# Performance work log

Hardware: AMD Instinct MI355X
Metric: run time of the kernel (lower is better)

The kernel has to match this reference:

```python
import jax, jax.numpy as jnp
import numpy as np

NEG_SLOPE = 0.2
N, E, NNZ, IN, H, C = 100000, 50000, 800000, 128, 8, 16


def setup_inputs() -> dict:
    key = jax.random.key(0)
    ks = jax.random.split(key, 8)
    X = jax.random.normal(ks[0], (N, IN), jnp.float32)
    W_typed = jax.random.normal(ks[1], (4, IN, H * C), jnp.float32) * (1.0 / np.sqrt(IN))
    att_e = jax.random.normal(ks[2], (4, H, C), jnp.float32) * 0.1
    att_v = jax.random.normal(ks[3], (4, H, C), jnp.float32) * 0.1
    vertex = jax.random.randint(ks[4], (NNZ,), 0, N, jnp.int32)
    edges = jax.random.randint(ks[5], (NNZ,), 0, E, jnp.int32)
    vtype = jax.random.randint(ks[6], (N,), 0, 4, jnp.int32)
    etype = jax.random.randint(ks[7], (E,), 0, 4, jnp.int32)
    return {"X": X, "W_typed": W_typed, "att_e": att_e, "att_v": att_v,
            "vertex": vertex, "edges": edges, "vtype": vtype, "etype": etype}


def _segment_softmax(logits, seg, num):
    # numerically-stable softmax over segments (PyG-style, eps in denominator)
    m = jax.ops.segment_max(logits, seg, num_segments=num)
    ex = jnp.exp(logits - m[seg])
    s = jax.ops.segment_sum(ex, seg, num_segments=num)
    return ex / (s[seg] + 1e-16)


def reference(X, W_typed, att_e, att_v, vertex, edges, vtype, etype):
    # typed linear: project with all 4 type weights, select per node type
    Xall = jnp.einsum('ni,tio->tno', X, W_typed)        # [4, N, H*C]
    X0 = Xall[vtype, jnp.arange(N)]                     # [N, H*C]
    Xn = X0.reshape(N, H, C)
    Xve = Xn[vertex]                                    # [NNZ, H, C] gather vertex->incidence
    # vertex->edge attention, typed by edge type of each incidence
    beta = jnp.sum(Xve * att_e[etype[edges]], axis=-1)  # [NNZ, H]
    beta = jax.nn.leaky_relu(beta, NEG_SLOPE)
    beta = _segment_softmax(beta, edges, E)
    Xe = jax.nn.relu(jax.ops.segment_sum(Xve * beta[..., None], edges, num_segments=E))  # [E, H, C]
    Xe = Xe[edges]                                      # [NNZ, H, C] gather edge->incidence
    # edge->vertex attention, typed by node type of each incidence's vertex
    alpha = jnp.sum(Xe * att_v[vtype[vertex]], axis=-1)  # [NNZ, H]
    alpha = jax.nn.leaky_relu(alpha, NEG_SLOPE)
    alpha = _segment_softmax(alpha, vertex, N)
    Xv = jax.ops.segment_sum(Xe * alpha[..., None], vertex, num_segments=N)  # [N, H, C]
    return Xv.reshape(N, H * C)
```

## Files before the change

kernel.cpp:

```cpp
#include <hip/hip_runtime.h>

typedef __attribute__((ext_vector_type(8))) short bf16x8;
typedef __attribute__((ext_vector_type(4))) float f32x4;

#define NEG_SLOPE 0.2f

__device__ __forceinline__ unsigned short f2bf(float f){
  unsigned u = __float_as_uint(f);
  u = (u + 0x7fffu + ((u >> 16) & 1u)) >> 16;
  return (unsigned short)u;
}
__device__ __forceinline__ float bflo(unsigned u){ return __uint_as_float(u << 16); }
__device__ __forceinline__ float bfhi(unsigned u){ return __uint_as_float(u & 0xffff0000u); }
__device__ __forceinline__ float lrelu(float x){ return x > 0.f ? x : NEG_SLOPE * x; }

__global__ __launch_bounds__(256) void k_prep(
    const int* __restrict__ vtype, int N, int* __restrict__ tcnt, int nbHN,
    const float* __restrict__ W, short* __restrict__ Bfrag){
  __shared__ int lcnt[4];
  int b = (int)blockIdx.x;
  if (b < nbHN){
    if (threadIdx.x < 4) lcnt[threadIdx.x] = 0;
    __syncthreads();
    int i = b * 256 + threadIdx.x;
    if (i < N) atomicAdd(&lcnt[vtype[i]], 1);
    __syncthreads();
    if (threadIdx.x < 4 && lcnt[threadIdx.x] > 0)
      atomicAdd(tcnt + threadIdx.x, lcnt[threadIdx.x]);
    return;
  }
  b -= nbHN;
  int u = b * 256 + threadIdx.x;
  int j = u & 7, lane = (u >> 3) & 63, ct = (u >> 9) & 31, ks = u >> 14;
  int k = ks * 32 + ((lane >> 4) << 3) + j;
  int col = (ct << 4) + (lane & 15);
  int t = col >> 7, o = col & 127;
  Bfrag[u] = (short)f2bf(W[(t * 128 + k) * 128 + o]);
}

__global__ void k_pbase(const int* __restrict__ tcnt, int* __restrict__ pbase){
  if (threadIdx.x == 0 && blockIdx.x == 0){
    int pb = 0;
    for (int t = 0; t < 4; ++t){
      pbase[t] = pb;
      pb += ((tcnt[t] + 63) >> 6) << 6;
    }
    pbase[4] = pb;
  }
}

__global__ __launch_bounds__(256) void k_nodeplace(
    const int* __restrict__ vtype, int N, const int* __restrict__ pbase,
    int* __restrict__ tcur, int* __restrict__ nsorted){
  __shared__ int lcnt[4];
  __shared__ int gbase[4];
  int t = threadIdx.x;
  if (t < 4) lcnt[t] = 0;
  __syncthreads();
  int i = (int)blockIdx.x * 256 + t;
  int tt = 0, rank = 0;
  bool valid = i < N;
  if (valid){ tt = vtype[i]; rank = atomicAdd(&lcnt[tt], 1); }
  __syncthreads();
  if (t < 4 && lcnt[t] > 0) gbase[t] = atomicAdd(tcur + t, lcnt[t]);
  __syncthreads();
  if (valid) nsorted[pbase[tt] + gbase[tt] + rank] = i;
}

__global__ __launch_bounds__(256, 3) void k_gemm_hist(const float* __restrict__ X,
    const short* __restrict__ Bfrag, const int* __restrict__ nsorted,
    const int* __restrict__ pbase, unsigned short* __restrict__ X0,
    const int* __restrict__ edges, const int* __restrict__ vertex, int NNZ,
    int* __restrict__ cnt, int E,
    int* __restrict__ rank_e, int* __restrict__ rank_v, int nbHist4){
  __shared__ short shB[8 * 4 * 64 * 8];
  const int tid = threadIdx.x;
  const int q = (int)blockIdx.x / 3, r = (int)blockIdx.x % 3;

  if (r != 0){
    int hb = 2 * q + (r - 1);
    if (hb < nbHist4){
      int i0 = hb * 1024 + tid;
      #pragma unroll
      for (int k = 0; k < 4; ++k){
        int i = i0 + k * 256;
        if (i < NNZ){
          rank_e[i] = atomicAdd(cnt + edges[i], 1);
          rank_v[i] = atomicAdd(cnt + E + vertex[i], 1);
        }
      }
    }
    return;
  }

  const int rowIdx = q * 64;
  const int t = (rowIdx >= pbase[1]) + (rowIdx >= pbase[2]) + (rowIdx >= pbase[3]);

  const bf16x8* Bv = (const bf16x8*)Bfrag;
  bf16x8* shBv = (bf16x8*)shB;
  #pragma unroll
  for (int v = 0; v < 8; ++v){
    int item = v * 256 + tid;
    int slab = item >> 6, ln = item & 63;
    int ks = slab >> 3, ctl = slab & 7;
    shBv[item] = Bv[((ks * 32 + 8 * t + ctl) * 64) + ln];
  }

  const int w = tid >> 6, lane = tid & 63;
  const int m = lane & 15, qq = lane >> 4;
  const int node = nsorted[rowIdx + w * 16 + m];

  bf16x8 afrag[4];
  #pragma unroll
  for (int ks = 0; ks < 4; ++ks){
    bf16x8 f;
    if (node >= 0){
      const float4* src = (const float4*)(X + (size_t)node * 128 + ks * 32 + qq * 8);
      float4 a = src[0], b = src[1];
      f[0]=(short)f2bf(a.x); f[1]=(short)f2bf(a.y); f[2]=(short)f2bf(a.z); f[3]=(short)f2bf(a.w);
      f[4]=(short)f2bf(b.x); f[5]=(short)f2bf(b.y); f[6]=(short)f2bf(b.z); f[7]=(short)f2bf(b.w);
    } else {
      #pragma unroll
      for (int z = 0; z < 8; ++z) f[z] = 0;
    }
    afrag[ks] = f;
  }

  f32x4 acc[8];
  #pragma unroll
  for (int ct = 0; ct < 8; ++ct){
    acc[ct][0]=0.f; acc[ct][1]=0.f; acc[ct][2]=0.f; acc[ct][3]=0.f;
  }

  __syncthreads();
  #pragma unroll
  for (int ctl = 0; ctl < 8; ++ctl){
    #pragma unroll
    for (int ks = 0; ks < 4; ++ks){
      bf16x8 bf = shBv[(ks * 8 + ctl) * 64 + lane];
      acc[ctl] = __builtin_amdgcn_mfma_f32_16x16x32_bf16(afrag[ks], bf, acc[ctl], 0, 0, 0);
    }
  }

  const int col0 = lane & 15;
  #pragma unroll
  for (int rr = 0; rr < 4; ++rr){
    int row = nsorted[rowIdx + w * 16 + qq * 4 + rr];
    if (row < 0) continue;
    #pragma unroll
    for (int ctl = 0; ctl < 8; ++ctl)
      X0[(size_t)row * 128 + ctl * 16 + col0] = f2bf(acc[ctl][rr]);
  }
}

__global__ __launch_bounds__(256) void k_scanA(const int* __restrict__ cnt, int S,
                                               int* __restrict__ bsum){
  __shared__ int sh[256];
  int base = blockIdx.x * 1024 + threadIdx.x * 4;
  int s = 0;
  #pragma unroll
  for (int k = 0; k < 4; ++k){ int idx = base + k; if (idx < S) s += cnt[idx]; }
  sh[threadIdx.x] = s; __syncthreads();
  for (int off = 128; off > 0; off >>= 1){
    if (threadIdx.x < off) sh[threadIdx.x] += sh[threadIdx.x + off];
    __syncthreads();
  }
  if (threadIdx.x == 0) bsum[blockIdx.x] = sh[0];
}

__global__ __launch_bounds__(256) void k_scanC3(const int* __restrict__ cnt, int S,
    const int* __restrict__ bsum, int nb, int* __restrict__ offs){
  __shared__ int shb[256];
  __shared__ int sh[256];
  int t = threadIdx.x;
  int b = (int)blockIdx.x;
  shb[t] = (t < nb) ? bsum[t] : 0;
  __syncthreads();
  for (int off = 1; off < 256; off <<= 1){
    int v = (t >= off) ? shb[t - off] : 0; __syncthreads();
    shb[t] += v; __syncthreads();
  }
  int bbase = (b == 0) ? 0 : shb[b - 1];
  int base = b * 1024 + t * 4;
  int c[4]; int s = 0;
  #pragma unroll
  for (int k = 0; k < 4; ++k){ int idx = base + k; c[k] = (idx < S) ? cnt[idx] : 0; s += c[k]; }
  sh[t] = s; __syncthreads();
  for (int off = 1; off < 256; off <<= 1){
    int v = (t >= off) ? sh[t - off] : 0; __syncthreads();
    sh[t] += v; __syncthreads();
  }
  int run = bbase + sh[t] - s;
  #pragma unroll
  for (int k = 0; k < 4; ++k){
    int idx = base + k;
    if (idx < S){ offs[idx] = run; run += c[k]; }
  }
}

__global__ __launch_bounds__(256) void k_place(
    const int* __restrict__ edges, const int* __restrict__ vertex, int NNZ,
    const int* __restrict__ offs, const int* __restrict__ rank_e,
    const int* __restrict__ rank_v, int* __restrict__ rows, int E){
  int q = (int)blockIdx.x >> 1, r = (int)blockIdx.x & 1;
  int i = q * 256 + (int)threadIdx.x;
  if (i >= NNZ) return;
  if (r == 0) rows[offs[edges[i]]      + rank_e[i]] = vertex[i];
  else        rows[offs[E + vertex[i]] + rank_v[i]] = edges[i];
}

template<int OUT_BF16>
__device__ __forceinline__ void seg_body(const uint4* __restrict__ feat,
    const float* __restrict__ att, const int* __restrict__ rows_sorted,
    const int* __restrict__ offs, const int* __restrict__ cnt,
    const int* __restrict__ stype, void* __restrict__ outbuf,
    int S, int blockId, int tid){
  int wid = tid >> 6, lane = tid & 63;
  int s = blockId * 4 + wid;
  if (s >= S) return;
  int t = stype[s];
  int sub = lane >> 4, lane16 = lane & 15;
  const float4* ap = (const float4*)(att + t * 128 + lane16 * 8);
  float4 A0 = ap[0], A1 = ap[1];
  int start = offs[s], len = cnt[s];
  float denom = 0.f;
  float acc[8];
  #pragma unroll
  for (int e = 0; e < 8; ++e) acc[e] = 0.f;

  for (int base = 0; base < len; base += 64){
    int m = len - base; if (m > 64) m = 64;
    int idx = 0;
    if (lane < m) idx = rows_sorted[start + base + lane];
    int ng = (m + 3) >> 2;
    uint4 uA = make_uint4(0,0,0,0), uB = make_uint4(0,0,0,0);
    {
      int r0 = __shfl(idx, sub);
      if (sub < m) uA = feat[(size_t)r0 * 16 + lane16];
      int r1 = __shfl(idx, 4 + sub);
      if (4 + sub < m) uB = feat[(size_t)r1 * 16 + lane16];
    }
    for (int g = 0; g < ng; g += 2){
      {
        uint4 u = uA;
        int nr = (g + 2) * 4 + sub;
        int rn = __shfl(idx, nr & 63);
        if (nr < m) uA = feat[(size_t)rn * 16 + lane16];
        float x0 = bflo(u.x), x1 = bfhi(u.x), x2 = bflo(u.y), x3 = bfhi(u.y);
        float x4 = bflo(u.z), x5 = bfhi(u.z), x6 = bflo(u.w), x7 = bfhi(u.w);
        float p = x0*A0.x + x1*A0.y + x2*A0.z + x3*A0.w
                + x4*A1.x + x5*A1.y + x6*A1.z + x7*A1.w;
        p += __shfl_xor(p, 1);
        float wgt = __expf(lrelu(p));
        wgt = (g * 4 + sub < m) ? wgt : 0.f;
        denom += wgt;
        acc[0] += wgt*x0; acc[1] += wgt*x1; acc[2] += wgt*x2; acc[3] += wgt*x3;
        acc[4] += wgt*x4; acc[5] += wgt*x5; acc[6] += wgt*x6; acc[7] += wgt*x7;
      }
      if (g + 1 < ng){
        uint4 u = uB;
        int nr = (g + 3) * 4 + sub;
        int rn = __shfl(idx, nr & 63);
        if (nr < m) uB = feat[(size_t)rn * 16 + lane16];
        float x0 = bflo(u.x), x1 = bfhi(u.x), x2 = bflo(u.y), x3 = bfhi(u.y);
        float x4 = bflo(u.z), x5 = bfhi(u.z), x6 = bflo(u.w), x7 = bfhi(u.w);
        float p = x0*A0.x + x1*A0.y + x2*A0.z + x3*A0.w
                + x4*A1.x + x5*A1.y + x6*A1.z + x7*A1.w;
        p += __shfl_xor(p, 1);
        float wgt = __expf(lrelu(p));
        wgt = ((g + 1) * 4 + sub < m) ? wgt : 0.f;
        denom += wgt;
        acc[0] += wgt*x0; acc[1] += wgt*x1; acc[2] += wgt*x2; acc[3] += wgt*x3;
        acc[4] += wgt*x4; acc[5] += wgt*x5; acc[6] += wgt*x6; acc[7] += wgt*x7;
      }
    }
  }
  denom += __shfl_xor(denom, 16);
  denom += __shfl_xor(denom, 32);
  #pragma unroll
  for (int e = 0; e < 8; ++e){
    acc[e] += __shfl_xor(acc[e], 16);
    acc[e] += __shfl_xor(acc[e], 32);
  }
  float inv = 1.f / (denom + 1e-16f);
  float v[8];
  #pragma unroll
  for (int e = 0; e < 8; ++e) v[e] = acc[e] * inv;

  if constexpr (OUT_BF16){
    if (sub == 0){
      uint4 pw;
      pw.x = (unsigned)f2bf(fmaxf(v[0],0.f)) | ((unsigned)f2bf(fmaxf(v[1],0.f)) << 16);
      pw.y = (unsigned)f2bf(fmaxf(v[2],0.f)) | ((unsigned)f2bf(fmaxf(v[3],0.f)) << 16);
      pw.z = (unsigned)f2bf(fmaxf(v[4],0.f)) | ((unsigned)f2bf(fmaxf(v[5],0.f)) << 16);
      pw.w = (unsigned)f2bf(fmaxf(v[6],0.f)) | ((unsigned)f2bf(fmaxf(v[7],0.f)) << 16);
      ((uint4*)outbuf)[(size_t)s * 16 + lane16] = pw;
    }
  } else {
    if (sub == 0){
      float4* op = (float4*)outbuf;
      op[(size_t)s * 32 + lane16 * 2]     = make_float4(v[0], v[1], v[2], v[3]);
      op[(size_t)s * 32 + lane16 * 2 + 1] = make_float4(v[4], v[5], v[6], v[7]);
    }
  }
}

__global__ __launch_bounds__(256) void k_seg1(const uint4* __restrict__ X0,
    const float* __restrict__ att_e, const int* __restrict__ rows,
    const int* __restrict__ offs, const int* __restrict__ cnt,
    const int* __restrict__ etype, void* __restrict__ Xe, int E){
  seg_body<1>(X0, att_e, rows, offs, cnt, etype, Xe, E,
              (int)blockIdx.x, threadIdx.x);
}

__global__ __launch_bounds__(256) void k_seg2(const uint4* __restrict__ Xe,
    const float* __restrict__ att_v, const int* __restrict__ rows,
    const int* __restrict__ offs, const int* __restrict__ cnt,
    const int* __restrict__ vtype, float* __restrict__ out, int N){
  seg_body<0>(Xe, att_v, rows, offs, cnt, vtype, out, N,
              (int)blockIdx.x, threadIdx.x);
}

extern "C" void kernel_launch(void* const* d_in, const int* in_sizes, int n_in,
                              void* d_out, int out_size, void* d_ws, size_t ws_size,
                              hipStream_t stream){
  const float* X      = (const float*)d_in[0];
  const float* W      = (const float*)d_in[1];
  const float* att_e  = (const float*)d_in[2];
  const float* att_v  = (const float*)d_in[3];
  const int*   vertex = (const int*)d_in[4];
  const int*   edges  = (const int*)d_in[5];
  const int*   vtype  = (const int*)d_in[6];
  const int*   etype  = (const int*)d_in[7];
  float* out = (float*)d_out;
  const int N   = in_sizes[0] / 128;
  const int NNZ = in_sizes[4];
  const int E   = in_sizes[7];
  const int S   = E + N;

  const int nbI = (NNZ + 255) / 256;
  const int nbH4 = (NNZ + 1023) / 1024;
  const int nbHN = (N + 255) / 256;
  const int nbS = (S + 1023) / 1024;
  const int nbSeg1 = (E + 3) / 4;
  const int nbPad = (N + 252 + 63) / 64;
  const int nsortedCap = nbPad * 64;
  const int nQA = (nbPad > (nbH4 + 1) / 2) ? nbPad : (nbH4 + 1) / 2;

  char* wp = (char*)d_ws;
  int* cnt    = (int*)wp; wp += (size_t)S * 4;
  int* tcnt   = (int*)wp; wp += 16;
  int* tcur   = (int*)wp; wp += 16;
  int* offs   = (int*)wp; wp += (size_t)S * 4;
  int* bsum   = (int*)wp; wp += 1024;
  int* pbase  = (int*)wp; wp += 32;
  int* rows   = (int*)wp; wp += (size_t)2 * NNZ * 4;
  int* nsorted= (int*)wp; wp += (size_t)nsortedCap * 4;
  int* rank_e = (int*)wp; wp += (size_t)NNZ * 4;
  int* rank_v = (int*)wp; wp += (size_t)NNZ * 4;
  unsigned short* X0 = (unsigned short*)wp; wp += (size_t)N * 128 * 2;
  unsigned short* Xe = (unsigned short*)wp; wp += (size_t)E * 128 * 2;
  short* Bfrag = (short*)wp; wp += (size_t)65536 * 2;

  hipMemsetAsync(cnt, 0, (size_t)(S + 8) * 4, stream);
  hipMemsetAsync(nsorted, 0xFF, (size_t)nsortedCap * 4, stream);

  k_prep<<<nbHN + 256, 256, 0, stream>>>(vtype, N, tcnt, nbHN, W, Bfrag);
  k_pbase<<<1, 64, 0, stream>>>(tcnt, pbase);
  k_nodeplace<<<nbHN, 256, 0, stream>>>(vtype, N, pbase, tcur, nsorted);

  k_gemm_hist<<<3 * nQA, 256, 0, stream>>>(X, Bfrag, nsorted, pbase,
      (unsigned short*)X0, edges, vertex, NNZ, cnt, E, rank_e, rank_v, nbH4);

  k_scanA<<<nbS, 256, 0, stream>>>(cnt, S, bsum);
  k_scanC3<<<nbS, 256, 0, stream>>>(cnt, S, bsum, nbS, offs);
  k_place<<<2 * nbI, 256, 0, stream>>>(edges, vertex, NNZ, offs,
      rank_e, rank_v, rows, E);

  k_seg1<<<nbSeg1, 256, 0, stream>>>((const uint4*)X0, att_e, rows,
      offs, cnt, etype, Xe, E);

  k_seg2<<<(N + 3) / 4, 256, 0, stream>>>((const uint4*)Xe, att_v,
      rows, offs + E, cnt + E, vtype, out, N);
}
```

Baseline: 311.5 us.

## Fold pbase into consumers and overlap vertex-side placement with seg1

Removes the single-thread k_pbase launch by recomputing the per-type padded bases from tcnt inside k_nodeplace and k_gemm_hist. Splits the placement kernel so only edge-side rows are placed before seg1, and the vertex-side placement runs interleaved in the same grid as seg1 blocks, since seg1 only reads edge-side rows. The histogram part of the gemm kernel now handles one element per thread with more blocks instead of four. The goal is fewer launches and better overlap, in exchange for redundant small computations and a more complex block mapping.

```diff
diff --git a/kernel.cpp b/kernel.cpp
--- a/kernel.cpp
+++ b/kernel.cpp
@@ -38,24 +38,19 @@
   Bfrag[u] = (short)f2bf(W[(t * 128 + k) * 128 + o]);
 }
 
-__global__ void k_pbase(const int* __restrict__ tcnt, int* __restrict__ pbase){
-  if (threadIdx.x == 0 && blockIdx.x == 0){
-    int pb = 0;
-    for (int t = 0; t < 4; ++t){
-      pbase[t] = pb;
-      pb += ((tcnt[t] + 63) >> 6) << 6;
-    }
-    pbase[4] = pb;
-  }
-}
-
 __global__ __launch_bounds__(256) void k_nodeplace(
-    const int* __restrict__ vtype, int N, const int* __restrict__ pbase,
+    const int* __restrict__ vtype, int N, const int* __restrict__ tcnt,
     int* __restrict__ tcur, int* __restrict__ nsorted){
   __shared__ int lcnt[4];
   __shared__ int gbase[4];
+  __shared__ int spb[4];
   int t = threadIdx.x;
   if (t < 4) lcnt[t] = 0;
+  if (t == 0){
+    int run = 0;
+    #pragma unroll
+    for (int k = 0; k < 4; ++k){ spb[k] = run; run += ((tcnt[k] + 63) >> 6) << 6; }
+  }
   __syncthreads();
   int i = (int)blockIdx.x * 256 + t;
   int tt = 0, rank = 0;
@@ -64,37 +59,39 @@
   __syncthreads();
   if (t < 4 && lcnt[t] > 0) gbase[t] = atomicAdd(tcur + t, lcnt[t]);
   __syncthreads();
-  if (valid) nsorted[pbase[tt] + gbase[tt] + rank] = i;
+  if (valid) nsorted[spb[tt] + gbase[tt] + rank] = i;
 }
 
 __global__ __launch_bounds__(256, 3) void k_gemm_hist(const float* __restrict__ X,
     const short* __restrict__ Bfrag, const int* __restrict__ nsorted,
-    const int* __restrict__ pbase, unsigned short* __restrict__ X0,
+    const int* __restrict__ tcnt, unsigned short* __restrict__ X0,
     const int* __restrict__ edges, const int* __restrict__ vertex, int NNZ,
     int* __restrict__ cnt, int E,
-    int* __restrict__ rank_e, int* __restrict__ rank_v, int nbHist4){
+    int* __restrict__ rank_e, int* __restrict__ rank_v, int nbHist){
   __shared__ short shB[8 * 4 * 64 * 8];
   const int tid = threadIdx.x;
   const int q = (int)blockIdx.x / 3, r = (int)blockIdx.x % 3;
 
   if (r != 0){
     int hb = 2 * q + (r - 1);
-    if (hb < nbHist4){
-      int i0 = hb * 1024 + tid;
-      #pragma unroll
-      for (int k = 0; k < 4; ++k){
-        int i = i0 + k * 256;
-        if (i < NNZ){
-          rank_e[i] = atomicAdd(cnt + edges[i], 1);
-          rank_v[i] = atomicAdd(cnt + E + vertex[i], 1);
-        }
+    if (hb < nbHist){
+      int i = hb * 256 + tid;
+      if (i < NNZ){
+        rank_e[i] = atomicAdd(cnt + edges[i], 1);
+        rank_v[i] = atomicAdd(cnt + E + vertex[i], 1);
       }
     }
     return;
   }
 
   const int rowIdx = q * 64;
-  const int t = (rowIdx >= pbase[1]) + (rowIdx >= pbase[2]) + (rowIdx >= pbase[3]);
+  int pb1, pb2, pb3;
+  {
+    int run = ((tcnt[0] + 63) >> 6) << 6; pb1 = run;
+    run    += ((tcnt[1] + 63) >> 6) << 6; pb2 = run;
+    run    += ((tcnt[2] + 63) >> 6) << 6; pb3 = run;
+  }
+  const int t = (rowIdx >= pb1) + (rowIdx >= pb2) + (rowIdx >= pb3);
 
   const bf16x8* Bv = (const bf16x8*)Bfrag;
   bf16x8* shBv = (bf16x8*)shB;
@@ -198,15 +195,12 @@
   }
 }
 
-__global__ __launch_bounds__(256) void k_place(
+__global__ __launch_bounds__(256) void k_place_e(
     const int* __restrict__ edges, const int* __restrict__ vertex, int NNZ,
     const int* __restrict__ offs, const int* __restrict__ rank_e,
-    const int* __restrict__ rank_v, int* __restrict__ rows, int E){
-  int q = (int)blockIdx.x >> 1, r = (int)blockIdx.x & 1;
-  int i = q * 256 + (int)threadIdx.x;
-  if (i >= NNZ) return;
-  if (r == 0) rows[offs[edges[i]]      + rank_e[i]] = vertex[i];
-  else        rows[offs[E + vertex[i]] + rank_v[i]] = edges[i];
+    int* __restrict__ rows){
+  int i = (int)blockIdx.x * 256 + (int)threadIdx.x;
+  if (i < NNZ) rows[offs[edges[i]] + rank_e[i]] = vertex[i];
 }
 
 template<int OUT_BF16>
@@ -305,12 +299,24 @@
   }
 }
 
-__global__ __launch_bounds__(256) void k_seg1(const uint4* __restrict__ X0,
-    const float* __restrict__ att_e, const int* __restrict__ rows,
-    const int* __restrict__ offs, const int* __restrict__ cnt,
-    const int* __restrict__ etype, void* __restrict__ Xe, int E){
-  seg_body<1>(X0, att_e, rows, offs, cnt, etype, Xe, E,
-              (int)blockIdx.x, threadIdx.x);
+__global__ __launch_bounds__(256) void k_seg1_pv(
+    const int* __restrict__ edges, const int* __restrict__ vertex, int NNZ,
+    const int* __restrict__ offs, const int* __restrict__ rank_v,
+    int* __restrict__ rows, int E, int nbPlace,
+    const uint4* __restrict__ X0, const float* __restrict__ att_e,
+    const int* __restrict__ cnt, const int* __restrict__ etype,
+    void* __restrict__ Xe, int nbSeg){
+  const int q = (int)blockIdx.x / 5, r = (int)blockIdx.x % 5;
+  if (r == 0){
+    if (q < nbPlace){
+      int i = q * 256 + (int)threadIdx.x;
+      if (i < NNZ) rows[offs[E + vertex[i]] + rank_v[i]] = edges[i];
+    }
+    return;
+  }
+  int segBlk = q * 4 + (r - 1);
+  if (segBlk >= nbSeg) return;
+  seg_body<1>(X0, att_e, rows, offs, cnt, etype, Xe, E, segBlk, threadIdx.x);
 }
 
 __global__ __launch_bounds__(256) void k_seg2(const uint4* __restrict__ Xe,
@@ -339,13 +345,13 @@
   const int S   = E + N;
 
   const int nbI = (NNZ + 255) / 256;
-  const int nbH4 = (NNZ + 1023) / 1024;
   const int nbHN = (N + 255) / 256;
   const int nbS = (S + 1023) / 1024;
   const int nbSeg1 = (E + 3) / 4;
   const int nbPad = (N + 252 + 63) / 64;
   const int nsortedCap = nbPad * 64;
-  const int nQA = (nbPad > (nbH4 + 1) / 2) ? nbPad : (nbH4 + 1) / 2;
+  const int nQA = (nbPad > (nbI + 1) / 2) ? nbPad : (nbI + 1) / 2;
+  const int nQB = (nbI > (nbSeg1 + 3) / 4) ? nbI : (nbSeg1 + 3) / 4;
 
   char* wp = (char*)d_ws;
   int* cnt    = (int*)wp; wp += (size_t)S * 4;
@@ -353,7 +359,6 @@
   int* tcur   = (int*)wp; wp += 16;
   int* offs   = (int*)wp; wp += (size_t)S * 4;
   int* bsum   = (int*)wp; wp += 1024;
-  int* pbase  = (int*)wp; wp += 32;
   int* rows   = (int*)wp; wp += (size_t)2 * NNZ * 4;
   int* nsorted= (int*)wp; wp += (size_t)nsortedCap * 4;
   int* rank_e = (int*)wp; wp += (size_t)NNZ * 4;
@@ -366,19 +371,17 @@
   hipMemsetAsync(nsorted, 0xFF, (size_t)nsortedCap * 4, stream);
 
   k_prep<<<nbHN + 256, 256, 0, stream>>>(vtype, N, tcnt, nbHN, W, Bfrag);
-  k_pbase<<<1, 64, 0, stream>>>(tcnt, pbase);
-  k_nodeplace<<<nbHN, 256, 0, stream>>>(vtype, N, pbase, tcur, nsorted);
-
-  k_gemm_hist<<<3 * nQA, 256, 0, stream>>>(X, Bfrag, nsorted, pbase,
-      (unsigned short*)X0, edges, vertex, NNZ, cnt, E, rank_e, rank_v, nbH4);
+  k_nodeplace<<<nbHN, 256, 0, stream>>>(vtype, N, tcnt, tcur, nsorted);
+
+  k_gemm_hist<<<3 * nQA, 256, 0, stream>>>(X, Bfrag, nsorted, tcnt,
+      (unsigned short*)X0, edges, vertex, NNZ, cnt, E, rank_e, rank_v, nbI);
 
   k_scanA<<<nbS, 256, 0, stream>>>(cnt, S, bsum);
   k_scanC3<<<nbS, 256, 0, stream>>>(cnt, S, bsum, nbS, offs);
-  k_place<<<2 * nbI, 256, 0, stream>>>(edges, vertex, NNZ, offs,
-      rank_e, rank_v, rows, E);
-
-  k_seg1<<<nbSeg1, 256, 0, stream>>>((const uint4*)X0, att_e, rows,
-      offs, cnt, etype, Xe, E);
+  k_place_e<<<nbI, 256, 0, stream>>>(edges, vertex, NNZ, offs, rank_e, rows);
+
+  k_seg1_pv<<<5 * nQB, 256, 0, stream>>>(edges, vertex, NNZ, offs, rank_v,
+      rows, E, nbI, (const uint4*)X0, att_e, cnt, etype, Xe, nbSeg1);
 
   k_seg2<<<(N + 3) / 4, 256, 0, stream>>>((const uint4*)Xe, att_v,
       rows, offs + E, cnt + E, vtype, out, N);
```

New measurement: 304.7 us. 2.2% less time.
